# Optimization experiments

Hardware: AMD Instinct MI355X
Metric: run time of the kernel (lower is better)

## Reference

```python
import jax, jax.numpy as jnp
import numpy as np

DIM = 32
HID = 128          # edge-MLP hidden width
N = 8192           # total nodes
E = 131072         # total edges
B = 64             # number of graphs
NUM_MP = 3
S2S_STEPS = 3


def setup_inputs() -> dict:
    key = jax.random.key(0)
    ks = jax.random.split(key, 24)
    g = lambda k, shape, s=0.05: jax.random.normal(k, shape, dtype=jnp.float32) * s

    inp = {
        "x": jax.random.normal(ks[0], (N, 1), dtype=jnp.float32),
        "edge_attr": jax.random.uniform(ks[1], (E, 2), dtype=jnp.float32),
        # params
        "lin0_w": g(ks[2], (1, DIM)), "lin0_b": g(ks[3], (DIM,)),
        "enn_w1": g(ks[4], (2, HID)), "enn_b1": g(ks[5], (HID,)),
        "enn_w2": g(ks[6], (HID, DIM * DIM)), "enn_b2": g(ks[7], (DIM * DIM,)),
        "root_w": g(ks[8], (DIM, DIM)), "conv_b": g(ks[9], (DIM,)),
        # GRU (gates ordered r,z,n as in torch)
        "gru_wih": g(ks[10], (DIM, 3 * DIM)), "gru_whh": g(ks[11], (DIM, 3 * DIM)),
        "gru_bih": g(ks[12], (3 * DIM,)), "gru_bhh": g(ks[13], (3 * DIM,)),
        # Set2Set LSTM: input 2*DIM, hidden DIM (gates ordered i,f,g,o as in torch)
        "s2s_wih": g(ks[14], (2 * DIM, 4 * DIM)), "s2s_whh": g(ks[15], (DIM, 4 * DIM)),
        "s2s_bih": g(ks[16], (4 * DIM,)), "s2s_bhh": g(ks[17], (4 * DIM,)),
        "lin1_w": g(ks[18], (2 * DIM, DIM)), "lin1_b": g(ks[19], (DIM,)),
        "lin2_w": g(ks[20], (DIM, 1)), "lin2_b": g(ks[21], (1,)),
        # int args
        "edge_index": jax.random.randint(ks[22], (2, E), 0, N, dtype=jnp.int32),
        "batch": jnp.sort(jax.random.randint(ks[23], (N,), 0, B, dtype=jnp.int32)),
    }
    return inp


def _forward(x, edge_attr, lin0_w, lin0_b, enn_w1, enn_b1, enn_w2, enn_b2,
             root_w, conv_b, gru_wih, gru_whh, gru_bih, gru_bhh,
             s2s_wih, s2s_whh, s2s_bih, s2s_bhh, lin1_w, lin1_b, lin2_w, lin2_b,
             edge_index, batch):
    src, dst = edge_index[0], edge_index[1]

    out = jax.nn.relu(x @ lin0_w + lin0_b)          # [N, DIM]
    h = out                                          # GRU hidden state

    # edge-conditioned weights (constant across MP layers -> hoisted)
    ew = jax.nn.relu(edge_attr @ enn_w1 + enn_b1) @ enn_w2 + enn_b2
    W = ew.reshape(E, DIM, DIM)                      # [E, in, out]

    deg = jnp.maximum(jax.ops.segment_sum(jnp.ones((E,), jnp.float32), dst,
                                          num_segments=N), 1.0)[:, None]

    for _ in range(NUM_MP):
        # NNConv: gather -> per-edge small matmul -> scatter-mean, + root + bias
        msg = jnp.einsum('ed,edo->eo', out[src], W)  # [E, DIM]
        agg = jax.ops.segment_sum(msg, dst, num_segments=N) / deg
        m = jax.nn.relu(agg + out @ root_w + conv_b)
        # GRU cell (single step)
        gi = m @ gru_wih + gru_bih
        gh = h @ gru_whh + gru_bhh
        ir, iz, in_ = jnp.split(gi, 3, axis=-1)
        hr, hz, hn = jnp.split(gh, 3, axis=-1)
        r = jax.nn.sigmoid(ir + hr)
        z = jax.nn.sigmoid(iz + hz)
        n = jnp.tanh(in_ + r * hn)
        h = (1.0 - z) * n + z * h
        out = h

    # Set2Set pooling
    qh = jnp.zeros((B, DIM), jnp.float32)
    qc = jnp.zeros((B, DIM), jnp.float32)
    q_star = jnp.zeros((B, 2 * DIM), jnp.float32)
    for _ in range(S2S_STEPS):
        gates = q_star @ s2s_wih + s2s_bih + qh @ s2s_whh + s2s_bhh
        i_, f_, g_, o_ = jnp.split(gates, 4, axis=-1)
        qc = jax.nn.sigmoid(f_) * qc + jax.nn.sigmoid(i_) * jnp.tanh(g_)
        qh = jax.nn.sigmoid(o_) * jnp.tanh(qc)       # [B, DIM]
        e = jnp.sum(out * qh[batch], axis=-1)        # [N] attention logits
        emax = jax.ops.segment_max(e, batch, num_segments=B)
        a = jnp.exp(e - emax[batch])
        a = a / jax.ops.segment_sum(a, batch, num_segments=B)[batch]
        r_read = jax.ops.segment_sum(a[:, None] * out, batch, num_segments=B)
        q_star = jnp.concatenate([qh, r_read], axis=-1)  # [B, 2*DIM]

    y = jax.nn.relu(q_star @ lin1_w + lin1_b) @ lin2_w + lin2_b
    return y.reshape(-1)                              # [B]


def reference(x, edge_attr, lin0_w, lin0_b, enn_w1, enn_b1, enn_w2, enn_b2,
              root_w, conv_b, gru_wih, gru_whh, gru_bih, gru_bhh,
              s2s_wih, s2s_whh, s2s_bih, s2s_bhh, lin1_w, lin1_b, lin2_w, lin2_b,
              edge_index, batch):
    return _forward(x, edge_attr, lin0_w, lin0_b, enn_w1, enn_b1, enn_w2, enn_b2,
                    root_w, conv_b, gru_wih, gru_whh, gru_bih, gru_bhh,
                    s2s_wih, s2s_whh, s2s_bih, s2s_bhh, lin1_w, lin1_b, lin2_w,
                    lin2_b, edge_index, batch)
```

## Files before the change

### kernel.cpp

```cpp
#include <hip/hip_runtime.h>

#define N_NODES 8192
#define N_EDGES 131072
#define NGRAPH  64
#define DIM     32
#define HID     128
#define KHALF   64
#define G_NODES 4
#define SROW    36

__device__ __forceinline__ float sigmoidf_(float x) { return 1.0f / (1.0f + expf(-x)); }

__global__ void prep1_kernel(const float* __restrict__ x, const float* __restrict__ w,
                             const float* __restrict__ b, float* __restrict__ out,
                             const int* __restrict__ dst, int* __restrict__ counts) {
  const int bb = blockIdx.x;
  if (bb < 1024) {
    int idx = bb * 256 + threadIdx.x;
    int n = idx >> 5, d = idx & 31;
    out[idx] = fmaxf(fmaf(x[n], w[d], b[d]), 0.0f);
  } else {
    int e = (bb - 1024) * 256 + threadIdx.x;
    atomicAdd(&counts[dst[e]], 1);
  }
}

__global__ void scan_kernel(const int* __restrict__ counts,
                            int* __restrict__ offsets,
                            float* __restrict__ deg_inv) {
  __shared__ int sm[1024];
  int t = threadIdx.x;
  int base = t * 8;
  int loc[8];
  int s = 0;
#pragma unroll
  for (int i = 0; i < 8; ++i) { loc[i] = s; s += counts[base + i]; }
  sm[t] = s;
  __syncthreads();
  for (int off = 1; off < 1024; off <<= 1) {
    int v = (t >= off) ? sm[t - off] : 0;
    __syncthreads();
    sm[t] += v;
    __syncthreads();
  }
  int excl = (t > 0) ? sm[t - 1] : 0;
#pragma unroll
  for (int i = 0; i < 8; ++i) {
    offsets[base + i] = excl + loc[i];
    int c = counts[base + i];
    deg_inv[base + i] = 1.0f / (float)(c > 0 ? c : 1);
  }
  if (t == 1023) offsets[N_NODES] = sm[1023];
}

__global__ void prep2_kernel(const int* __restrict__ ei, const float* __restrict__ ea,
                             const int* __restrict__ offsets, int* __restrict__ cursor,
                             int* __restrict__ csr_src, float2* __restrict__ csr_ea,
                             const int* __restrict__ batch, int* __restrict__ gstart) {
  const int bb = blockIdx.x;
  if (bb < 512) {
    int e = bb * 256 + threadIdx.x;
    int d = ei[N_EDGES + e];
    int pos = atomicAdd(&cursor[d], 1);
    int slot = offsets[d] + pos;
    csr_src[slot] = ei[e];
    csr_ea[slot] = make_float2(ea[2 * e], ea[2 * e + 1]);
  } else {
    int n = (bb - 512) * 256 + threadIdx.x;
    int b = batch[n];
    if (n == 0) {
      for (int g = 0; g <= b; ++g) gstart[g] = 0;
    } else {
      int bp = batch[n - 1];
      for (int g = bp + 1; g <= b; ++g) gstart[g] = n;
    }
    if (n == N_NODES - 1) {
      for (int g = b + 1; g <= NGRAPH; ++g) gstart[g] = N_NODES;
    }
  }
}

__global__ __launch_bounds__(256, 4) void mp_half_kernel(
    const float* __restrict__ out_cur, const int* __restrict__ offsets,
    const int* __restrict__ csr_src, const float2* __restrict__ csr_ea,
    const float* __restrict__ w1, const float* __restrict__ b1,
    const float* __restrict__ w2, float* __restrict__ partial,
    float* __restrict__ O) {
  constexpr int C = 32;
  __shared__ float smem[G_NODES * KHALF * SROW];
  float* S = smem;
  float* hidb = smem;
  float* osrcb = smem + C * KHALF;
  float* red = smem;
  __shared__ int offs[G_NODES + 1];

  const int t = threadIdx.x;
  const int bb = blockIdx.x;
  const int khalf = bb & 1;
  const int node0 = (bb >> 1) * G_NODES;

  if (t <= G_NODES) offs[t] = offsets[min(node0 + t, N_NODES)];

  const int kg = t >> 4, dg = t & 15;
  const int k0 = kg * 4, d0 = dg * 2;
  const int ec = t >> 3, sub = t & 7;

  float w1x[8], w1y[8], b1v[8];
#pragma unroll
  for (int i = 0; i < 8; ++i) {
    const int kgl = khalf * KHALF + sub * 8 + i;
    w1x[i] = w1[kgl];
    w1y[i] = w1[HID + kgl];
    b1v[i] = b1[kgl];
  }

  float acc[G_NODES][4][2];
#pragma unroll
  for (int g = 0; g < G_NODES; ++g)
#pragma unroll
    for (int i = 0; i < 4; ++i) { acc[g][i][0] = 0.0f; acc[g][i][1] = 0.0f; }
  float oacc[G_NODES] = {};
  __syncthreads();

#pragma unroll
  for (int g = 0; g < G_NODES; ++g) {
    const int base = offs[g], end = offs[g + 1];
    for (int c0 = base; c0 < end; c0 += C) {
      const int cnt = min(C, end - c0);
      __syncthreads();
      if (ec < cnt) {
        const int slot = c0 + ec;
        const float2 eav = csr_ea[slot];
        const int sidx = csr_src[slot];
        float hv[8];
#pragma unroll
        for (int i = 0; i < 8; ++i)
          hv[i] = fmaxf(fmaf(eav.y, w1y[i], fmaf(eav.x, w1x[i], b1v[i])), 0.0f);
        *(float4*)(hidb + ec * KHALF + sub * 8) =
            make_float4(hv[0], hv[1], hv[2], hv[3]);
        *(float4*)(hidb + ec * KHALF + sub * 8 + 4) =
            make_float4(hv[4], hv[5], hv[6], hv[7]);
        *(float4*)(osrcb + ec * DIM + sub * 4) =
            *(const float4*)(out_cur + sidx * DIM + sub * 4);
      }
      __syncthreads();
      for (int e = 0; e < cnt; ++e) {
        const float4 hvv = *(const float4*)(hidb + e * KHALF + k0);
        const float2 ov = *(const float2*)(osrcb + e * DIM + d0);
        acc[g][0][0] = fmaf(hvv.x, ov.x, acc[g][0][0]);
        acc[g][0][1] = fmaf(hvv.x, ov.y, acc[g][0][1]);
        acc[g][1][0] = fmaf(hvv.y, ov.x, acc[g][1][0]);
        acc[g][1][1] = fmaf(hvv.y, ov.y, acc[g][1][1]);
        acc[g][2][0] = fmaf(hvv.z, ov.x, acc[g][2][0]);
        acc[g][2][1] = fmaf(hvv.z, ov.y, acc[g][2][1]);
        acc[g][3][0] = fmaf(hvv.w, ov.x, acc[g][3][0]);
        acc[g][3][1] = fmaf(hvv.w, ov.y, acc[g][3][1]);
        if (khalf == 0 && t < DIM) oacc[g] += osrcb[e * DIM + t];
      }
    }
  }
  __syncthreads();

  {
    const int shift = (kg & 3) * 8;
    const int dd = (d0 + shift) & 31;
#pragma unroll
    for (int g = 0; g < G_NODES; ++g) {
      float* Sg = S + g * KHALF * SROW;
#pragma unroll
      for (int i = 0; i < 4; ++i)
        *(float2*)(Sg + (k0 + i) * SROW + dd) = make_float2(acc[g][i][0], acc[g][i][1]);
    }
  }
  if (khalf == 0 && t < DIM) {
#pragma unroll
    for (int g = 0; g < G_NODES; ++g) {
      const int node = node0 + g;
      if (node < N_NODES) O[node * DIM + t] = oacc[g];
    }
  }
  __syncthreads();

  {
    const int ks = t >> 4;
    const int dvh = (t >> 3) & 1;
    const int og = t & 7;
    const int shift = (ks & 3) * 8;
    float a4[G_NODES][4];
#pragma unroll
    for (int g = 0; g < G_NODES; ++g)
#pragma unroll
      for (int r = 0; r < 4; ++r) a4[g][r] = 0.0f;
#pragma unroll
    for (int i = 0; i < 4; ++i) {
      const int kl = ks * 4 + i;
      const float* w2k = w2 + (size_t)(khalf * KHALF + kl) * (DIM * DIM);
#pragma unroll
      for (int q = 0; q < 4; ++q) {
        const int dbase = dvh * 16 + q * 4;
        const int dq = (dbase + shift) & 31;
        const float4 sv0 = *(const float4*)(S + 0 * KHALF * SROW + kl * SROW + dq);
        const float4 sv1 = *(const float4*)(S + 1 * KHALF * SROW + kl * SROW + dq);
        const float4 sv2 = *(const float4*)(S + 2 * KHALF * SROW + kl * SROW + dq);
        const float4 sv3 = *(const float4*)(S + 3 * KHALF * SROW + kl * SROW + dq);
        const float* s0 = (const float*)&sv0;
        const float* s1 = (const float*)&sv1;
        const float* s2 = (const float*)&sv2;
        const float* s3 = (const float*)&sv3;
#pragma unroll
        for (int r = 0; r < 4; ++r) {
          const float4 wv = *(const float4*)(w2k + (dbase + r) * DIM + og * 4);
          a4[0][0] = fmaf(s0[r], wv.x, a4[0][0]);
          a4[0][1] = fmaf(s0[r], wv.y, a4[0][1]);
          a4[0][2] = fmaf(s0[r], wv.z, a4[0][2]);
          a4[0][3] = fmaf(s0[r], wv.w, a4[0][3]);
          a4[1][0] = fmaf(s1[r], wv.x, a4[1][0]);
          a4[1][1] = fmaf(s1[r], wv.y, a4[1][1]);
          a4[1][2] = fmaf(s1[r], wv.z, a4[1][2]);
          a4[1][3] = fmaf(s1[r], wv.w, a4[1][3]);
          a4[2][0] = fmaf(s2[r], wv.x, a4[2][0]);
          a4[2][1] = fmaf(s2[r], wv.y, a4[2][1]);
          a4[2][2] = fmaf(s2[r], wv.z, a4[2][2]);
          a4[2][3] = fmaf(s2[r], wv.w, a4[2][3]);
          a4[3][0] = fmaf(s3[r], wv.x, a4[3][0]);
          a4[3][1] = fmaf(s3[r], wv.y, a4[3][1]);
          a4[3][2] = fmaf(s3[r], wv.z, a4[3][2]);
          a4[3][3] = fmaf(s3[r], wv.w, a4[3][3]);
        }
      }
    }
    __syncthreads();
#pragma unroll
    for (int g = 0; g < G_NODES; ++g)
#pragma unroll
      for (int r = 0; r < 4; ++r) red[(g * 4 + r) * 257 + t] = a4[g][r];
  }
  __syncthreads();
  if (t < G_NODES * DIM) {
    const int g = t >> 5, o = t & 31;
    const int og = o >> 2, r = o & 3;
    const float* rp = red + (g * 4 + r) * 257 + og;
    float sum = 0.0f;
#pragma unroll
    for (int j = 0; j < 32; ++j) sum += rp[j * 8];
    const int node = node0 + g;
    if (node < N_NODES)
      partial[(size_t)khalf * N_NODES * DIM + node * DIM + o] = sum;
  }
}

__global__ __launch_bounds__(256) void epilogue_kernel(
    const float* __restrict__ partial, const float* __restrict__ O,
    const float* __restrict__ out_cur, const float* __restrict__ b2,
    const float* __restrict__ deg_inv, const float* __restrict__ root_w,
    const float* __restrict__ conv_b, const float* __restrict__ gwih,
    const float* __restrict__ gwhh, const float* __restrict__ gbih,
    const float* __restrict__ gbhh, float* __restrict__ out_nxt) {
  __shared__ float hb[256], ob[256], mb[256], b2s[1024];
  const int t = threadIdx.x;
  const int node0 = blockIdx.x * 8;
  hb[t] = out_cur[node0 * DIM + t];
  ob[t] = O[node0 * DIM + t];
#pragma unroll
  for (int i = 0; i < 4; ++i) b2s[i * 256 + t] = b2[i * 256 + t];
  __syncthreads();
  const int g = t >> 5, o = t & 31;
  const int node = node0 + g;
  float agg = partial[node * DIM + o] +
              partial[(size_t)N_NODES * DIM + node * DIM + o];
#pragma unroll
  for (int d = 0; d < DIM; ++d) agg = fmaf(ob[g * DIM + d], b2s[d * DIM + o], agg);
  agg *= deg_inv[node];
  float rt = conv_b[o];
#pragma unroll
  for (int d = 0; d < DIM; ++d) rt = fmaf(hb[g * DIM + d], root_w[d * DIM + o], rt);
  mb[t] = fmaxf(agg + rt, 0.0f);
  __syncthreads();
  float gi[3], gh[3];
#pragma unroll
  for (int jj = 0; jj < 3; ++jj) {
    float si = gbih[jj * DIM + o], sh = gbhh[jj * DIM + o];
#pragma unroll
    for (int d = 0; d < DIM; ++d) {
      si = fmaf(mb[g * DIM + d], gwih[d * 3 * DIM + jj * DIM + o], si);
      sh = fmaf(hb[g * DIM + d], gwhh[d * 3 * DIM + jj * DIM + o], sh);
    }
    gi[jj] = si;
    gh[jj] = sh;
  }
  const float r = sigmoidf_(gi[0] + gh[0]);
  const float z = sigmoidf_(gi[1] + gh[1]);
  const float nn = tanhf(fmaf(r, gh[2], gi[2]));
  out_nxt[node * DIM + o] = (1.0f - z) * nn + z * hb[t];
}

__global__ __launch_bounds__(256) void s2s_kernel(
    const float* __restrict__ outf, const int* __restrict__ gstart,
    const float* __restrict__ wih, const float* __restrict__ whh,
    const float* __restrict__ bih, const float* __restrict__ bhh,
    const float* __restrict__ l1w, const float* __restrict__ l1b,
    const float* __restrict__ l2w, const float* __restrict__ l2b,
    float* __restrict__ y) {
  __shared__ float qh[DIM], qc[DIM], qstar[2 * DIM], gates[4 * DIM];
  __shared__ float wsum[4], wmax[4], wr[4][DIM];
  const int b = blockIdx.x, t = threadIdx.x;
  const int gs = gstart[b], ge = gstart[b + 1];
  const int w = t >> 6, lane = t & 63;
  if (t < DIM) { qh[t] = 0.0f; qc[t] = 0.0f; }
  if (t < 2 * DIM) qstar[t] = 0.0f;
  __syncthreads();
  for (int step = 0; step < 3; ++step) {
    if (t < 4 * DIM) {
      float gv = bih[t] + bhh[t];
      for (int i = 0; i < 2 * DIM; ++i) gv = fmaf(qstar[i], wih[i * 4 * DIM + t], gv);
      for (int i = 0; i < DIM; ++i) gv = fmaf(qh[i], whh[i * 4 * DIM + t], gv);
      gates[t] = gv;
    }
    __syncthreads();
    if (t < DIM) {
      const float ig = sigmoidf_(gates[t]);
      const float fg = sigmoidf_(gates[DIM + t]);
      const float gg = tanhf(gates[2 * DIM + t]);
      const float og = sigmoidf_(gates[3 * DIM + t]);
      const float c = fmaf(fg, qc[t], ig * gg);
      qc[t] = c;
      qh[t] = og * tanhf(c);
    }
    __syncthreads();
    float lmax = -INFINITY;
    for (int n = gs + t; n < ge; n += 256) {
      const float* orow = outf + n * DIM;
      float e = 0.0f;
#pragma unroll
      for (int d = 0; d < DIM; ++d) e = fmaf(orow[d], qh[d], e);
      lmax = fmaxf(lmax, e);
    }
#pragma unroll
    for (int off = 32; off > 0; off >>= 1) lmax = fmaxf(lmax, __shfl_xor(lmax, off));
    if (lane == 0) wmax[w] = lmax;
    __syncthreads();
    const float gmax = fmaxf(fmaxf(wmax[0], wmax[1]), fmaxf(wmax[2], wmax[3]));
    float rl[DIM];
#pragma unroll
    for (int d = 0; d < DIM; ++d) rl[d] = 0.0f;
    float lsum = 0.0f;
    for (int n = gs + t; n < ge; n += 256) {
      const float* orow = outf + n * DIM;
      float e = 0.0f;
#pragma unroll
      for (int d = 0; d < DIM; ++d) e = fmaf(orow[d], qh[d], e);
      const float a = expf(e - gmax);
      lsum += a;
#pragma unroll
      for (int d = 0; d < DIM; ++d) rl[d] = fmaf(a, orow[d], rl[d]);
    }
#pragma unroll
    for (int off = 32; off > 0; off >>= 1) {
      lsum += __shfl_xor(lsum, off);
#pragma unroll
      for (int d = 0; d < DIM; ++d) rl[d] += __shfl_xor(rl[d], off);
    }
    __syncthreads();
    if (lane == 0) {
      wsum[w] = lsum;
#pragma unroll
      for (int d = 0; d < DIM; ++d) wr[w][d] = rl[d];
    }
    __syncthreads();
    if (t < DIM) {
      const float stot = wsum[0] + wsum[1] + wsum[2] + wsum[3];
      const float rv = wr[0][t] + wr[1][t] + wr[2][t] + wr[3][t];
      qstar[t] = qh[t];
      qstar[DIM + t] = (stot > 0.0f) ? rv / stot : 0.0f;
    }
    __syncthreads();
  }
  if (t < DIM) {
    float u = l1b[t];
    for (int i = 0; i < 2 * DIM; ++i) u = fmaf(qstar[i], l1w[i * DIM + t], u);
    u = fmaxf(u, 0.0f);
    float v = u * l2w[t];
#pragma unroll
    for (int off = 16; off > 0; off >>= 1) v += __shfl_xor(v, off);
    if (t == 0) y[b] = v + l2b[0];
  }
}

extern "C" void kernel_launch(void* const* d_in, const int* in_sizes, int n_in,
                              void* d_out, int out_size, void* d_ws, size_t ws_size,
                              hipStream_t stream) {
  const float* x        = (const float*)d_in[0];
  const float* ea       = (const float*)d_in[1];
  const float* lin0_w   = (const float*)d_in[2];
  const float* lin0_b   = (const float*)d_in[3];
  const float* enn_w1   = (const float*)d_in[4];
  const float* enn_b1   = (const float*)d_in[5];
  const float* enn_w2   = (const float*)d_in[6];
  const float* enn_b2   = (const float*)d_in[7];
  const float* root_w   = (const float*)d_in[8];
  const float* conv_b   = (const float*)d_in[9];
  const float* gru_wih  = (const float*)d_in[10];
  const float* gru_whh  = (const float*)d_in[11];
  const float* gru_bih  = (const float*)d_in[12];
  const float* gru_bhh  = (const float*)d_in[13];
  const float* s2s_wih  = (const float*)d_in[14];
  const float* s2s_whh  = (const float*)d_in[15];
  const float* s2s_bih  = (const float*)d_in[16];
  const float* s2s_bhh  = (const float*)d_in[17];
  const float* lin1_w   = (const float*)d_in[18];
  const float* lin1_b   = (const float*)d_in[19];
  const float* lin2_w   = (const float*)d_in[20];
  const float* lin2_b   = (const float*)d_in[21];
  const int*   ei       = (const int*)d_in[22];
  const int*   batch    = (const int*)d_in[23];
  float* y = (float*)d_out;

  char* p = (char*)d_ws;
  auto alloc = [&](size_t bytes) -> void* {
    void* r = (void*)p;
    p += (bytes + 255) & ~(size_t)255;
    return r;
  };
  float*  out_a   = (float*)alloc(N_NODES * DIM * 4);
  float*  out_b   = (float*)alloc(N_NODES * DIM * 4);
  int*    counts  = (int*)alloc(N_NODES * 4);
  int*    offsets = (int*)alloc((N_NODES + 1) * 4);
  int*    cursor  = (int*)alloc(N_NODES * 4);
  int*    csr_src = (int*)alloc(N_EDGES * 4);
  float2* csr_ea  = (float2*)alloc(N_EDGES * 8);
  float*  deg_inv = (float*)alloc(N_NODES * 4);
  int*    gstart  = (int*)alloc((NGRAPH + 1) * 4);
  float*  Obuf    = (float*)alloc((size_t)N_NODES * DIM * 4);
  float*  partial = (float*)alloc((size_t)2 * N_NODES * DIM * 4);
  (void)ws_size; (void)n_in; (void)in_sizes; (void)out_size;

  hipMemsetAsync(counts, 0, N_NODES * 4, stream);
  hipMemsetAsync(cursor, 0, N_NODES * 4, stream);

  prep1_kernel<<<1024 + 512, 256, 0, stream>>>(x, lin0_w, lin0_b, out_a,
                                               ei + N_EDGES, counts);
  scan_kernel<<<1, 1024, 0, stream>>>(counts, offsets, deg_inv);
  prep2_kernel<<<512 + 32, 256, 0, stream>>>(ei, ea, offsets, cursor, csr_src,
                                             csr_ea, batch, gstart);

  const int ngroups = (N_NODES + G_NODES - 1) / G_NODES;
  const float* cur = out_a;
  float* nxt = out_b;
  for (int layer = 0; layer < 3; ++layer) {
    mp_half_kernel<<<ngroups * 2, 256, 0, stream>>>(
        cur, offsets, csr_src, csr_ea, enn_w1, enn_b1, enn_w2, partial, Obuf);
    epilogue_kernel<<<N_NODES / 8, 256, 0, stream>>>(
        partial, Obuf, cur, enn_b2, deg_inv, root_w, conv_b,
        gru_wih, gru_whh, gru_bih, gru_bhh, nxt);
    const float* tmp = cur; cur = nxt; nxt = (float*)tmp;
  }

  s2s_kernel<<<NGRAPH, 256, 0, stream>>>(cur, gstart, s2s_wih, s2s_whh, s2s_bih,
                                         s2s_bhh, lin1_w, lin1_b, lin2_w, lin2_b, y);
}
```

Baseline: 416.8 us.

## Merge per-node edge chunks and prefetch next chunk's gathers into registers

The edge loop now walks the whole contiguous CSR range of the block's nodes in shared chunks instead of chunking each node separately, which cuts partially filled chunks and barrier pairs. It also software-pipelines the gather: the next chunk's src index, edge attributes and source row are loaded into registers while the current chunk is being accumulated, hiding global-memory latency. The cost is extra register pressure and per-node range clipping inside each chunk.

```diff
diff --git a/kernel.cpp b/kernel.cpp
--- a/kernel.cpp
+++ b/kernel.cpp
@@ -122,29 +122,50 @@
   float oacc[G_NODES] = {};
   __syncthreads();
 
-#pragma unroll
-  for (int g = 0; g < G_NODES; ++g) {
-    const int base = offs[g], end = offs[g + 1];
-    for (int c0 = base; c0 < end; c0 += C) {
-      const int cnt = min(C, end - c0);
-      __syncthreads();
-      if (ec < cnt) {
-        const int slot = c0 + ec;
-        const float2 eav = csr_ea[slot];
-        const int sidx = csr_src[slot];
-        float hv[8];
-#pragma unroll
-        for (int i = 0; i < 8; ++i)
-          hv[i] = fmaxf(fmaf(eav.y, w1y[i], fmaf(eav.x, w1x[i], b1v[i])), 0.0f);
-        *(float4*)(hidb + ec * KHALF + sub * 8) =
-            make_float4(hv[0], hv[1], hv[2], hv[3]);
-        *(float4*)(hidb + ec * KHALF + sub * 8 + 4) =
-            make_float4(hv[4], hv[5], hv[6], hv[7]);
-        *(float4*)(osrcb + ec * DIM + sub * 4) =
-            *(const float4*)(out_cur + sidx * DIM + sub * 4);
-      }
-      __syncthreads();
-      for (int e = 0; e < cnt; ++e) {
+  const int tbeg = offs[0], tend = offs[G_NODES];
+
+  int cur0 = tbeg;
+  bool act = (ec < tend - cur0);
+  int sidx0 = 0;
+  float2 eav0 = make_float2(0.0f, 0.0f);
+  float4 orow0 = make_float4(0.0f, 0.0f, 0.0f, 0.0f);
+  if (act) {
+    sidx0 = csr_src[cur0 + ec];
+    eav0 = csr_ea[cur0 + ec];
+  }
+  if (act) orow0 = *(const float4*)(out_cur + sidx0 * DIM + sub * 4);
+
+  for (int c0 = tbeg; c0 < tend; c0 += C) {
+    const int cend = min(c0 + C, tend);
+    const int cn0 = c0 + C;
+    const bool actn = (ec < tend - cn0);
+    int sidx1 = 0;
+    float2 eav1 = make_float2(0.0f, 0.0f);
+    if (actn) {
+      sidx1 = csr_src[cn0 + ec];
+      eav1 = csr_ea[cn0 + ec];
+    }
+    __syncthreads();
+    if (act) {
+      float hv[8];
+#pragma unroll
+      for (int i = 0; i < 8; ++i)
+        hv[i] = fmaxf(fmaf(eav0.y, w1y[i], fmaf(eav0.x, w1x[i], b1v[i])), 0.0f);
+      *(float4*)(hidb + ec * KHALF + sub * 8) =
+          make_float4(hv[0], hv[1], hv[2], hv[3]);
+      *(float4*)(hidb + ec * KHALF + sub * 8 + 4) =
+          make_float4(hv[4], hv[5], hv[6], hv[7]);
+      *(float4*)(osrcb + ec * DIM + sub * 4) = orow0;
+    }
+    __syncthreads();
+    float4 orow1 = make_float4(0.0f, 0.0f, 0.0f, 0.0f);
+    if (actn) orow1 = *(const float4*)(out_cur + sidx1 * DIM + sub * 4);
+
+#pragma unroll
+    for (int g = 0; g < G_NODES; ++g) {
+      const int lo = max(offs[g], c0) - c0;
+      const int hi = min(offs[g + 1], cend) - c0;
+      for (int e = lo; e < hi; ++e) {
         const float4 hvv = *(const float4*)(hidb + e * KHALF + k0);
         const float2 ov = *(const float2*)(osrcb + e * DIM + d0);
         acc[g][0][0] = fmaf(hvv.x, ov.x, acc[g][0][0]);
@@ -158,6 +179,10 @@
         if (khalf == 0 && t < DIM) oacc[g] += osrcb[e * DIM + t];
       }
     }
+    act = actn;
+    sidx0 = sidx1;
+    eav0 = eav1;
+    orow0 = orow1;
   }
   __syncthreads();
 
```

New measurement: 427.8 us. +2.6%, slower.

## Fuse preprocessing kernels and memsets into one cooperative grid-synced kernel

Applied to the files above, without the earlier changes.

Replaces two memsets and three preprocessing launches (lin0, degree count, scan, CSR build) with a single cooperative kernel of 64 blocks x 1024 threads that uses grid.sync between phases. This removes launch and inter-kernel gaps for the small setup work. In exchange the kernel runs on only 64 blocks, the scan still runs serially in one block while the others wait at the barrier, and cooperative launch adds its own cost. The fused kernel relies on all 64 blocks being co-resident on the device.

```diff
diff --git a/kernel.cpp b/kernel.cpp
--- a/kernel.cpp
+++ b/kernel.cpp
@@ -1,4 +1,7 @@
 #include <hip/hip_runtime.h>
+#include <hip/hip_cooperative_groups.h>
+
+namespace cg = cooperative_groups;
 
 #define N_NODES 8192
 #define N_EDGES 131072
@@ -11,71 +14,85 @@
 
 __device__ __forceinline__ float sigmoidf_(float x) { return 1.0f / (1.0f + expf(-x)); }
 
-__global__ void prep1_kernel(const float* __restrict__ x, const float* __restrict__ w,
-                             const float* __restrict__ b, float* __restrict__ out,
-                             const int* __restrict__ dst, int* __restrict__ counts) {
-  const int bb = blockIdx.x;
-  if (bb < 1024) {
-    int idx = bb * 256 + threadIdx.x;
-    int n = idx >> 5, d = idx & 31;
-    out[idx] = fmaxf(fmaf(x[n], w[d], b[d]), 0.0f);
-  } else {
-    int e = (bb - 1024) * 256 + threadIdx.x;
-    atomicAdd(&counts[dst[e]], 1);
-  }
-}
-
-__global__ void scan_kernel(const int* __restrict__ counts,
-                            int* __restrict__ offsets,
-                            float* __restrict__ deg_inv) {
+__global__ __launch_bounds__(1024) void prep_fused_kernel(
+    const float* __restrict__ x, const float* __restrict__ lin0_w,
+    const float* __restrict__ lin0_b, float* __restrict__ out,
+    const int* __restrict__ ei, const float* __restrict__ ea,
+    const int* __restrict__ batch,
+    int* __restrict__ counts, int* __restrict__ offsets,
+    int* __restrict__ cursor, int* __restrict__ csr_src,
+    float2* __restrict__ csr_ea, float* __restrict__ deg_inv,
+    int* __restrict__ gstart) {
   __shared__ int sm[1024];
-  int t = threadIdx.x;
-  int base = t * 8;
-  int loc[8];
-  int s = 0;
-#pragma unroll
-  for (int i = 0; i < 8; ++i) { loc[i] = s; s += counts[base + i]; }
-  sm[t] = s;
-  __syncthreads();
-  for (int off = 1; off < 1024; off <<= 1) {
-    int v = (t >= off) ? sm[t - off] : 0;
-    __syncthreads();
-    sm[t] += v;
-    __syncthreads();
-  }
-  int excl = (t > 0) ? sm[t - 1] : 0;
-#pragma unroll
-  for (int i = 0; i < 8; ++i) {
-    offsets[base + i] = excl + loc[i];
-    int c = counts[base + i];
-    deg_inv[base + i] = 1.0f / (float)(c > 0 ? c : 1);
-  }
-  if (t == 1023) offsets[N_NODES] = sm[1023];
-}
-
-__global__ void prep2_kernel(const int* __restrict__ ei, const float* __restrict__ ea,
-                             const int* __restrict__ offsets, int* __restrict__ cursor,
-                             int* __restrict__ csr_src, float2* __restrict__ csr_ea,
-                             const int* __restrict__ batch, int* __restrict__ gstart) {
-  const int bb = blockIdx.x;
-  if (bb < 512) {
-    int e = bb * 256 + threadIdx.x;
-    int d = ei[N_EDGES + e];
-    int pos = atomicAdd(&cursor[d], 1);
-    int slot = offsets[d] + pos;
-    csr_src[slot] = ei[e];
-    csr_ea[slot] = make_float2(ea[2 * e], ea[2 * e + 1]);
-  } else {
-    int n = (bb - 512) * 256 + threadIdx.x;
-    int b = batch[n];
-    if (n == 0) {
-      for (int g = 0; g <= b; ++g) gstart[g] = 0;
-    } else {
-      int bp = batch[n - 1];
-      for (int g = bp + 1; g <= b; ++g) gstart[g] = n;
-    }
-    if (n == N_NODES - 1) {
-      for (int g = b + 1; g <= NGRAPH; ++g) gstart[g] = N_NODES;
+  cg::grid_group grid = cg::this_grid();
+  const int gt = blockIdx.x * 1024 + threadIdx.x;
+
+  if (gt < N_NODES) { counts[gt] = 0; cursor[gt] = 0; }
+#pragma unroll
+  for (int i = 0; i < 4; ++i) {
+    const int idx = gt * 4 + i;
+    const int n = idx >> 5, d = idx & 31;
+    out[idx] = fmaxf(fmaf(x[n], lin0_w[d], lin0_b[d]), 0.0f);
+  }
+  grid.sync();
+
+  {
+    const int* dst = ei + N_EDGES;
+    const int e0 = gt * 2;
+    atomicAdd(&counts[dst[e0]], 1);
+    atomicAdd(&counts[dst[e0 + 1]], 1);
+  }
+  grid.sync();
+
+  if (blockIdx.x == 0) {
+    const int t = threadIdx.x;
+    const int base = t * 8;
+    int loc[8];
+    int s = 0;
+#pragma unroll
+    for (int i = 0; i < 8; ++i) { loc[i] = s; s += counts[base + i]; }
+    sm[t] = s;
+    __syncthreads();
+    for (int off = 1; off < 1024; off <<= 1) {
+      int v = (t >= off) ? sm[t - off] : 0;
+      __syncthreads();
+      sm[t] += v;
+      __syncthreads();
+    }
+    const int excl = (t > 0) ? sm[t - 1] : 0;
+#pragma unroll
+    for (int i = 0; i < 8; ++i) {
+      offsets[base + i] = excl + loc[i];
+      const int c = counts[base + i];
+      deg_inv[base + i] = 1.0f / (float)(c > 0 ? c : 1);
+    }
+    if (t == 1023) offsets[N_NODES] = sm[1023];
+  }
+  grid.sync();
+
+  {
+    const int e0 = gt * 2;
+#pragma unroll
+    for (int k = 0; k < 2; ++k) {
+      const int e = e0 + k;
+      const int d = ei[N_EDGES + e];
+      const int pos = atomicAdd(&cursor[d], 1);
+      const int slot = offsets[d] + pos;
+      csr_src[slot] = ei[e];
+      csr_ea[slot] = make_float2(ea[2 * e], ea[2 * e + 1]);
+    }
+    if (gt < N_NODES) {
+      const int n = gt;
+      const int b = batch[n];
+      if (n == 0) {
+        for (int g = 0; g <= b; ++g) gstart[g] = 0;
+      } else {
+        const int bp = batch[n - 1];
+        for (int g = bp + 1; g <= b; ++g) gstart[g] = n;
+      }
+      if (n == N_NODES - 1) {
+        for (int g = b + 1; g <= NGRAPH; ++g) gstart[g] = N_NODES;
+      }
     }
   }
 }
@@ -434,14 +451,13 @@
   float*  partial = (float*)alloc((size_t)2 * N_NODES * DIM * 4);
   (void)ws_size; (void)n_in; (void)in_sizes; (void)out_size;
 
-  hipMemsetAsync(counts, 0, N_NODES * 4, stream);
-  hipMemsetAsync(cursor, 0, N_NODES * 4, stream);
-
-  prep1_kernel<<<1024 + 512, 256, 0, stream>>>(x, lin0_w, lin0_b, out_a,
-                                               ei + N_EDGES, counts);
-  scan_kernel<<<1, 1024, 0, stream>>>(counts, offsets, deg_inv);
-  prep2_kernel<<<512 + 32, 256, 0, stream>>>(ei, ea, offsets, cursor, csr_src,
-                                             csr_ea, batch, gstart);
+  void* prep_args[] = {
+      (void*)&x, (void*)&lin0_w, (void*)&lin0_b, (void*)&out_a,
+      (void*)&ei, (void*)&ea, (void*)&batch,
+      (void*)&counts, (void*)&offsets, (void*)&cursor,
+      (void*)&csr_src, (void*)&csr_ea, (void*)&deg_inv, (void*)&gstart};
+  hipLaunchCooperativeKernel((void*)prep_fused_kernel, dim3(64), dim3(1024),
+                             prep_args, 0, stream);
 
   const int ngroups = (N_NODES + G_NODES - 1) / G_NODES;
   const float* cur = out_a;
```

Result: slower. 486.1 us (+16.6%).

## Fuse full-K message passing with GRU epilogue into one kernel per layer

Applied to the files above, without the earlier changes.

Replaces the two-block-per-node-group split over the hidden dimension with a single block covering all 128 hidden units, and folds the epilogue (bias aggregation, root transform, GRU update) into the same kernel. This removes the partial/O global buffers, one kernel launch per layer, and the duplicated gather and edge-MLP work done by both K-halves. In exchange there are half as many blocks, more registers per thread (launch bounds 2), and larger shared memory, which lowers occupancy.

```diff
diff --git a/kernel.cpp b/kernel.cpp
--- a/kernel.cpp
+++ b/kernel.cpp
@@ -5,7 +5,7 @@
 #define NGRAPH  64
 #define DIM     32
 #define HID     128
-#define KHALF   64
+#define KFULL   128
 #define G_NODES 4
 #define SROW    36
 
@@ -80,45 +80,52 @@
   }
 }
 
-__global__ __launch_bounds__(256, 4) void mp_half_kernel(
+__global__ __launch_bounds__(256, 2) void mp_full_kernel(
     const float* __restrict__ out_cur, const int* __restrict__ offsets,
     const int* __restrict__ csr_src, const float2* __restrict__ csr_ea,
     const float* __restrict__ w1, const float* __restrict__ b1,
-    const float* __restrict__ w2, float* __restrict__ partial,
-    float* __restrict__ O) {
+    const float* __restrict__ w2, const float* __restrict__ b2,
+    const float* __restrict__ deg_inv, const float* __restrict__ root_w,
+    const float* __restrict__ conv_b, const float* __restrict__ gwih,
+    const float* __restrict__ gwhh, const float* __restrict__ gbih,
+    const float* __restrict__ gbhh, float* __restrict__ out_nxt) {
   constexpr int C = 32;
-  __shared__ float smem[G_NODES * KHALF * SROW];
+  __shared__ float smem[G_NODES * KFULL * SROW];
   float* S = smem;
   float* hidb = smem;
-  float* osrcb = smem + C * KHALF;
+  float* osrcb = smem + C * KFULL;
   float* red = smem;
+  float* ob  = smem + 4352;
+  float* hb  = smem + 4480;
+  float* mb  = smem + 4608;
+  float* b2s = smem + 4736;
   __shared__ int offs[G_NODES + 1];
 
   const int t = threadIdx.x;
-  const int bb = blockIdx.x;
-  const int khalf = bb & 1;
-  const int node0 = (bb >> 1) * G_NODES;
-
-  if (t <= G_NODES) offs[t] = offsets[min(node0 + t, N_NODES)];
-
-  const int kg = t >> 4, dg = t & 15;
-  const int k0 = kg * 4, d0 = dg * 2;
+  const int node0 = blockIdx.x * G_NODES;
+
+  if (t <= G_NODES) offs[t] = offsets[node0 + t];
+
+  const int kg = t >> 3, dg = t & 7;
+  const int k0 = kg * 4, d0 = dg * 4;
   const int ec = t >> 3, sub = t & 7;
 
-  float w1x[8], w1y[8], b1v[8];
-#pragma unroll
-  for (int i = 0; i < 8; ++i) {
-    const int kgl = khalf * KHALF + sub * 8 + i;
+  float w1x[16], w1y[16], b1v[16];
+#pragma unroll
+  for (int i = 0; i < 16; ++i) {
+    const int kgl = sub * 16 + i;
     w1x[i] = w1[kgl];
     w1y[i] = w1[HID + kgl];
     b1v[i] = b1[kgl];
   }
 
-  float acc[G_NODES][4][2];
+  float acc[G_NODES][4][4];
 #pragma unroll
   for (int g = 0; g < G_NODES; ++g)
 #pragma unroll
-    for (int i = 0; i < 4; ++i) { acc[g][i][0] = 0.0f; acc[g][i][1] = 0.0f; }
+    for (int i = 0; i < 4; ++i)
+#pragma unroll
+      for (int j = 0; j < 4; ++j) acc[g][i][j] = 0.0f;
   float oacc[G_NODES] = {};
   __syncthreads();
 
@@ -132,30 +139,38 @@
         const int slot = c0 + ec;
         const float2 eav = csr_ea[slot];
         const int sidx = csr_src[slot];
-        float hv[8];
-#pragma unroll
-        for (int i = 0; i < 8; ++i)
+        float hv[16];
+#pragma unroll
+        for (int i = 0; i < 16; ++i)
           hv[i] = fmaxf(fmaf(eav.y, w1y[i], fmaf(eav.x, w1x[i], b1v[i])), 0.0f);
-        *(float4*)(hidb + ec * KHALF + sub * 8) =
-            make_float4(hv[0], hv[1], hv[2], hv[3]);
-        *(float4*)(hidb + ec * KHALF + sub * 8 + 4) =
-            make_float4(hv[4], hv[5], hv[6], hv[7]);
+#pragma unroll
+        for (int j = 0; j < 4; ++j)
+          *(float4*)(hidb + ec * KFULL + sub * 16 + j * 4) =
+              make_float4(hv[j * 4], hv[j * 4 + 1], hv[j * 4 + 2], hv[j * 4 + 3]);
         *(float4*)(osrcb + ec * DIM + sub * 4) =
             *(const float4*)(out_cur + sidx * DIM + sub * 4);
       }
       __syncthreads();
       for (int e = 0; e < cnt; ++e) {
-        const float4 hvv = *(const float4*)(hidb + e * KHALF + k0);
-        const float2 ov = *(const float2*)(osrcb + e * DIM + d0);
+        const float4 hvv = *(const float4*)(hidb + e * KFULL + k0);
+        const float4 ov = *(const float4*)(osrcb + e * DIM + d0);
         acc[g][0][0] = fmaf(hvv.x, ov.x, acc[g][0][0]);
         acc[g][0][1] = fmaf(hvv.x, ov.y, acc[g][0][1]);
+        acc[g][0][2] = fmaf(hvv.x, ov.z, acc[g][0][2]);
+        acc[g][0][3] = fmaf(hvv.x, ov.w, acc[g][0][3]);
         acc[g][1][0] = fmaf(hvv.y, ov.x, acc[g][1][0]);
         acc[g][1][1] = fmaf(hvv.y, ov.y, acc[g][1][1]);
+        acc[g][1][2] = fmaf(hvv.y, ov.z, acc[g][1][2]);
+        acc[g][1][3] = fmaf(hvv.y, ov.w, acc[g][1][3]);
         acc[g][2][0] = fmaf(hvv.z, ov.x, acc[g][2][0]);
         acc[g][2][1] = fmaf(hvv.z, ov.y, acc[g][2][1]);
+        acc[g][2][2] = fmaf(hvv.z, ov.z, acc[g][2][2]);
+        acc[g][2][3] = fmaf(hvv.z, ov.w, acc[g][2][3]);
         acc[g][3][0] = fmaf(hvv.w, ov.x, acc[g][3][0]);
         acc[g][3][1] = fmaf(hvv.w, ov.y, acc[g][3][1]);
-        if (khalf == 0 && t < DIM) oacc[g] += osrcb[e * DIM + t];
+        acc[g][3][2] = fmaf(hvv.w, ov.z, acc[g][3][2]);
+        acc[g][3][3] = fmaf(hvv.w, ov.w, acc[g][3][3]);
+        if (t < DIM) oacc[g] += osrcb[e * DIM + t];
       }
     }
   }
@@ -166,17 +181,11 @@
     const int dd = (d0 + shift) & 31;
 #pragma unroll
     for (int g = 0; g < G_NODES; ++g) {
-      float* Sg = S + g * KHALF * SROW;
+      float* Sg = S + g * KFULL * SROW;
 #pragma unroll
       for (int i = 0; i < 4; ++i)
-        *(float2*)(Sg + (k0 + i) * SROW + dd) = make_float2(acc[g][i][0], acc[g][i][1]);
-    }
-  }
-  if (khalf == 0 && t < DIM) {
-#pragma unroll
-    for (int g = 0; g < G_NODES; ++g) {
-      const int node = node0 + g;
-      if (node < N_NODES) O[node * DIM + t] = oacc[g];
+        *(float4*)(Sg + (k0 + i) * SROW + dd) =
+            make_float4(acc[g][i][0], acc[g][i][1], acc[g][i][2], acc[g][i][3]);
     }
   }
   __syncthreads();
@@ -185,24 +194,25 @@
     const int ks = t >> 4;
     const int dvh = (t >> 3) & 1;
     const int og = t & 7;
-    const int shift = (ks & 3) * 8;
     float a4[G_NODES][4];
 #pragma unroll
     for (int g = 0; g < G_NODES; ++g)
 #pragma unroll
       for (int r = 0; r < 4; ++r) a4[g][r] = 0.0f;
 #pragma unroll
-    for (int i = 0; i < 4; ++i) {
-      const int kl = ks * 4 + i;
-      const float* w2k = w2 + (size_t)(khalf * KHALF + kl) * (DIM * DIM);
+    for (int i = 0; i < 8; ++i) {
+      const int kl = ks * 8 + i;
+      const int shift = ((kl >> 2) & 3) * 8;
+      const float* w2k = w2 + (size_t)kl * (DIM * DIM);
 #pragma unroll
       for (int q = 0; q < 4; ++q) {
         const int dbase = dvh * 16 + q * 4;
         const int dq = (dbase + shift) & 31;
-        const float4 sv0 = *(const float4*)(S + 0 * KHALF * SROW + kl * SROW + dq);
-        const float4 sv1 = *(const float4*)(S + 1 * KHALF * SROW + kl * SROW + dq);
-        const float4 sv2 = *(const float4*)(S + 2 * KHALF * SROW + kl * SROW + dq);
-        const float4 sv3 = *(const float4*)(S + 3 * KHALF * SROW + kl * SROW + dq);
+        const int soff = kl * SROW + dq;
+        const float4 sv0 = *(const float4*)(S + 0 * KFULL * SROW + soff);
+        const float4 sv1 = *(const float4*)(S + 1 * KFULL * SROW + soff);
+        const float4 sv2 = *(const float4*)(S + 2 * KFULL * SROW + soff);
+        const float4 sv3 = *(const float4*)(S + 3 * KFULL * SROW + soff);
         const float* s0 = (const float*)&sv0;
         const float* s1 = (const float*)&sv1;
         const float* s2 = (const float*)&sv2;
@@ -235,63 +245,50 @@
 #pragma unroll
       for (int r = 0; r < 4; ++r) red[(g * 4 + r) * 257 + t] = a4[g][r];
   }
-  __syncthreads();
+  if (t < DIM) {
+#pragma unroll
+    for (int g = 0; g < G_NODES; ++g) ob[g * DIM + t] = oacc[g];
+  }
+  if (t < G_NODES * DIM) hb[t] = out_cur[node0 * DIM + t];
+#pragma unroll
+  for (int i = 0; i < 4; ++i) b2s[i * 256 + t] = b2[i * 256 + t];
+  __syncthreads();
+
   if (t < G_NODES * DIM) {
     const int g = t >> 5, o = t & 31;
-    const int og = o >> 2, r = o & 3;
-    const float* rp = red + (g * 4 + r) * 257 + og;
-    float sum = 0.0f;
-#pragma unroll
-    for (int j = 0; j < 32; ++j) sum += rp[j * 8];
-    const int node = node0 + g;
-    if (node < N_NODES)
-      partial[(size_t)khalf * N_NODES * DIM + node * DIM + o] = sum;
-  }
-}
-
-__global__ __launch_bounds__(256) void epilogue_kernel(
-    const float* __restrict__ partial, const float* __restrict__ O,
-    const float* __restrict__ out_cur, const float* __restrict__ b2,
-    const float* __restrict__ deg_inv, const float* __restrict__ root_w,
-    const float* __restrict__ conv_b, const float* __restrict__ gwih,
-    const float* __restrict__ gwhh, const float* __restrict__ gbih,
-    const float* __restrict__ gbhh, float* __restrict__ out_nxt) {
-  __shared__ float hb[256], ob[256], mb[256], b2s[1024];
-  const int t = threadIdx.x;
-  const int node0 = blockIdx.x * 8;
-  hb[t] = out_cur[node0 * DIM + t];
-  ob[t] = O[node0 * DIM + t];
-#pragma unroll
-  for (int i = 0; i < 4; ++i) b2s[i * 256 + t] = b2[i * 256 + t];
-  __syncthreads();
-  const int g = t >> 5, o = t & 31;
-  const int node = node0 + g;
-  float agg = partial[node * DIM + o] +
-              partial[(size_t)N_NODES * DIM + node * DIM + o];
-#pragma unroll
-  for (int d = 0; d < DIM; ++d) agg = fmaf(ob[g * DIM + d], b2s[d * DIM + o], agg);
-  agg *= deg_inv[node];
-  float rt = conv_b[o];
-#pragma unroll
-  for (int d = 0; d < DIM; ++d) rt = fmaf(hb[g * DIM + d], root_w[d * DIM + o], rt);
-  mb[t] = fmaxf(agg + rt, 0.0f);
-  __syncthreads();
-  float gi[3], gh[3];
-#pragma unroll
-  for (int jj = 0; jj < 3; ++jj) {
-    float si = gbih[jj * DIM + o], sh = gbhh[jj * DIM + o];
-#pragma unroll
-    for (int d = 0; d < DIM; ++d) {
-      si = fmaf(mb[g * DIM + d], gwih[d * 3 * DIM + jj * DIM + o], si);
-      sh = fmaf(hb[g * DIM + d], gwhh[d * 3 * DIM + jj * DIM + o], sh);
-    }
-    gi[jj] = si;
-    gh[jj] = sh;
-  }
-  const float r = sigmoidf_(gi[0] + gh[0]);
-  const float z = sigmoidf_(gi[1] + gh[1]);
-  const float nn = tanhf(fmaf(r, gh[2], gi[2]));
-  out_nxt[node * DIM + o] = (1.0f - z) * nn + z * hb[t];
+    const int og2 = o >> 2, r2 = o & 3;
+    const float* rp = red + (g * 4 + r2) * 257 + og2;
+    float agg = 0.0f;
+#pragma unroll
+    for (int j = 0; j < 32; ++j) agg += rp[j * 8];
+#pragma unroll
+    for (int d = 0; d < DIM; ++d) agg = fmaf(ob[g * DIM + d], b2s[d * DIM + o], agg);
+    agg *= deg_inv[node0 + g];
+    float rt = conv_b[o];
+#pragma unroll
+    for (int d = 0; d < DIM; ++d) rt = fmaf(hb[g * DIM + d], root_w[d * DIM + o], rt);
+    mb[t] = fmaxf(agg + rt, 0.0f);
+  }
+  __syncthreads();
+  if (t < G_NODES * DIM) {
+    const int g = t >> 5, o = t & 31;
+    float gi[3], gh[3];
+#pragma unroll
+    for (int jj = 0; jj < 3; ++jj) {
+      float si = gbih[jj * DIM + o], sh = gbhh[jj * DIM + o];
+#pragma unroll
+      for (int d = 0; d < DIM; ++d) {
+        si = fmaf(mb[g * DIM + d], gwih[d * 3 * DIM + jj * DIM + o], si);
+        sh = fmaf(hb[g * DIM + d], gwhh[d * 3 * DIM + jj * DIM + o], sh);
+      }
+      gi[jj] = si;
+      gh[jj] = sh;
+    }
+    const float r = sigmoidf_(gi[0] + gh[0]);
+    const float z = sigmoidf_(gi[1] + gh[1]);
+    const float nn = tanhf(fmaf(r, gh[2], gi[2]));
+    out_nxt[(node0 * DIM) + t] = (1.0f - z) * nn + z * hb[t];
+  }
 }
 
 __global__ __launch_bounds__(256) void s2s_kernel(
@@ -430,8 +427,6 @@
   float2* csr_ea  = (float2*)alloc(N_EDGES * 8);
   float*  deg_inv = (float*)alloc(N_NODES * 4);
   int*    gstart  = (int*)alloc((NGRAPH + 1) * 4);
-  float*  Obuf    = (float*)alloc((size_t)N_NODES * DIM * 4);
-  float*  partial = (float*)alloc((size_t)2 * N_NODES * DIM * 4);
   (void)ws_size; (void)n_in; (void)in_sizes; (void)out_size;
 
   hipMemsetAsync(counts, 0, N_NODES * 4, stream);
@@ -443,15 +438,13 @@
   prep2_kernel<<<512 + 32, 256, 0, stream>>>(ei, ea, offsets, cursor, csr_src,
                                              csr_ea, batch, gstart);
 
-  const int ngroups = (N_NODES + G_NODES - 1) / G_NODES;
+  const int ngroups = N_NODES / G_NODES;
   const float* cur = out_a;
   float* nxt = out_b;
   for (int layer = 0; layer < 3; ++layer) {
-    mp_half_kernel<<<ngroups * 2, 256, 0, stream>>>(
-        cur, offsets, csr_src, csr_ea, enn_w1, enn_b1, enn_w2, partial, Obuf);
-    epilogue_kernel<<<N_NODES / 8, 256, 0, stream>>>(
-        partial, Obuf, cur, enn_b2, deg_inv, root_w, conv_b,
-        gru_wih, gru_whh, gru_bih, gru_bhh, nxt);
+    mp_full_kernel<<<ngroups, 256, 0, stream>>>(
+        cur, offsets, csr_src, csr_ea, enn_w1, enn_b1, enn_w2, enn_b2,
+        deg_inv, root_w, conv_b, gru_wih, gru_whh, gru_bih, gru_bhh, nxt);
     const float* tmp = cur; cur = nxt; nxt = (float*)tmp;
   }
 
```

After: 444.1 us. +6.6%, slower.
